# Kernel optimization log

Hardware: AMD Instinct MI355X
Metric: run time of the kernel (lower is better)

Reference implementation:

```python
import jax, jax.numpy as jnp
import numpy as np

MAX_NUM_CENTERS = 100
CENTER_IGNORE_PX = 3
SIGMA = 2.0   # center_gt_blur
KSIZE = 21    # GaussianLayer kernel size (ReflectionPad2d(10) + Conv2d(k=21))


def _gauss_kernel():
    r = KSIZE // 2
    x = jnp.arange(-r, r + 1, dtype=jnp.float32)
    g = jnp.exp(-0.5 * (x / SIGMA) ** 2)
    g = g / g.sum()
    return jnp.outer(g, g)  # [21,21], sums to 1 (matches scipy gaussian_filter of a delta)


def _gaussian_blur(x):
    # x: [B,H,W] -> depthwise 21x21 gaussian with reflect padding (GaussianLayer)
    r = KSIZE // 2
    k = _gauss_kernel()[None, None]  # [1,1,21,21]
    xp = jnp.pad(x[:, None], ((0, 0), (0, 0), (r, r), (r, r)), mode="reflect")
    y = jax.lax.conv_general_dilated(xp, k, (1, 1), "VALID",
                                     dimension_numbers=("NCHW", "OIHW", "NCHW"))
    return y[:, 0]


def setup_inputs() -> dict:
    key = jax.random.key(0)
    k1, k2 = jax.random.split(key)
    B, H, W = 8, 768, 768
    instances = jax.random.randint(k1, (B, 1, H, W), 0, MAX_NUM_CENTERS, dtype=jnp.int32)
    centers = jax.random.uniform(k2, (B, MAX_NUM_CENTERS, 2), dtype=jnp.float32) * (H - 1) + 1.0
    return {"instances": instances, "centers": centers}


def reference(instances, centers):
    B, _, H, W = instances.shape
    inst = instances[:, 0]                                # [B,H,W]
    col = jnp.arange(W, dtype=jnp.float32)                # xym_s[0][i,j] = j
    row = jnp.arange(H, dtype=jnp.float32)[:, None]       # xym_s[1][i,j] = i

    valid = inst > 0                                      # instance_mask
    has_inst = jnp.any(valid, axis=(1, 2)).astype(jnp.float32)  # len(unique)>1 gate

    # per-pixel nearest-center gather: center = centers[b, id-1]
    idx = jnp.clip(inst - 1, 0, MAX_NUM_CENTERS - 1)
    c = centers[jnp.arange(B)[:, None, None], idx]        # [B,H,W,2]
    gt_cx = jnp.where(valid, c[..., 1], -10000.0)         # gt_center_x (swapped coords)
    gt_cy = jnp.where(valid, c[..., 0], -10000.0)

    gt_X = gt_cx - row                                    # gt_center_x - xym_s[1]
    gt_Y = gt_cy - col                                    # gt_center_y - xym_s[0]

    near = (jnp.abs(gt_X) < CENTER_IGNORE_PX) & (jnp.abs(gt_Y) < CENTER_IGNORE_PX)
    # batches with no instances skip the block -> ignore stays all-ones
    ignore = jnp.where(has_inst[:, None, None] > 0, (~near).astype(jnp.float32), 1.0)

    m = valid.astype(jnp.float32)
    R = jnp.sqrt(gt_X ** 2 + gt_Y ** 2) * m
    theta_raw = jnp.arctan2(gt_Y, gt_X)
    theta = theta_raw * has_inst[:, None, None]           # skipped (zero) when no instances
    s = jnp.sin(theta_raw) * m
    cth = jnp.cos(theta_raw) * m
    M = jnp.sqrt(s ** 2 + cth ** 2)                       # == m, kept for faithfulness
    s = jnp.where(valid, s / jnp.maximum(M, 1e-12), 0.0)
    cth = jnp.where(valid, cth / jnp.maximum(M, 1e-12), 0.0)

    # gt_center_mask: zeros if no center-neighborhood pixels, else normalized blur
    blur = _gaussian_blur(1.0 - ignore)
    all_ones = jnp.all(ignore >= 1.0, axis=(1, 2))        # gt_center_mask.all()
    bmax = jnp.max(blur, axis=(1, 2), keepdims=True)
    cmask = jnp.where(all_ones[:, None, None], 0.0, blur / jnp.maximum(bmax, 1e-12))

    top = jnp.stack([R, theta, s, cth, ignore, cmask], axis=1)       # [B,6,H,W]
    mat = jnp.concatenate([top, jnp.zeros((B, 7, H, W), top.dtype)], axis=1)[:, :, None]
    # mat: [B,13,1,H,W]; channels 6..12 are zero (no orientation input)

    # gt_centers[id] = centers[b, id-1][[1,0]] for each instance id present
    present = jnp.zeros((B, MAX_NUM_CENTERS), dtype=bool).at[
        jnp.arange(B)[:, None], inst.reshape(B, -1)].set(True)
    swapped = centers[..., ::-1]
    gt_centers = jnp.zeros_like(centers).at[:, 1:, :].set(
        jnp.where(present[:, 1:, None], swapped[:, :-1, :], 0.0))

    return mat, gt_centers
```

## Files before the change

### kernel.cpp

```cpp
#include <hip/hip_runtime.h>
#include <math.h>

#define NB 8
#define NH 768
#define NW 768
#define NHW (NH*NW)
#define NCEN 100
#define NPIX (NB*NHW)
#define RAD 10
#define KS 21

#define SCAN_BLKS (NPIX / 4096)
#define BLKS_PER_B (NHW / 4096)
#define LIST_CAP 4096
#define QBLK_PER_B (NHW / 1024)
#define CAND_BLKS 96
#define FCAP 1024

#define HDR_HAS 0
#define HDR_CNT 8
#define HDR_BMAX 16
#define HDR_MASK 24
#define HDR_LIST 64

typedef float f4 __attribute__((ext_vector_type(4)));

__device__ const float g_G[KS] = {
    7.4335e-7f, 7.9919e-6f, 6.6915e-5f, 0.00043634f, 0.00221592f,
    0.00876415f, 0.02699548f, 0.06475880f, 0.12098536f, 0.17603266f,
    0.19947114f,
    0.17603266f, 0.12098536f, 0.06475880f, 0.02699548f, 0.00876415f,
    0.00221592f, 0.00043634f, 6.6915e-5f, 7.9919e-6f, 7.4335e-7f};

__device__ __forceinline__ float wfun(int p, int q, const float* __restrict__ g) {
    int d = p - q;
    float w = 0.f;
    if (d >= -RAD && d <= RAD) w = g[d + RAD];
    int a = p + q;
    if (q > 0 && a <= RAD) w += g[a + RAD];
    if (q < NH - 1 && a >= 2 * (NH - 1) - RAD) w += g[a - 2 * (NH - 1) + RAD];
    return w;
}

__device__ __forceinline__ float fatan2(float Y, float X) {
    float ax = fabsf(X), ay = fabsf(Y);
    float mx = fmaxf(ax, ay), mn = fminf(ax, ay);
    float a = mx > 0.f ? __fdividef(mn, mx) : 0.f;
    float ss = a * a;
    float r = fmaf(fmaf(fmaf(fmaf(fmaf(-0.01172120f, ss, 0.05265332f), ss,
                -0.11643287f), ss, 0.19354346f), ss, -0.33262347f), ss, 0.99997726f) * a;
    if (ay > ax) r = 1.57079637f - r;
    if (X < 0.f) r = 3.14159274f - r;
    return copysignf(r, Y);
}

__global__ void k_init(int* __restrict__ hdr) {
    if (threadIdx.x < 64) hdr[threadIdx.x] = 0;
}

__global__ __launch_bounds__(256) void k_scan(const int4* __restrict__ inst4,
                                              const float* __restrict__ centers,
                                              int* __restrict__ hdr) {
    __shared__ unsigned sm[4];
    __shared__ float2 s_c2[NCEN];
    int t = threadIdx.x;
    int blk = blockIdx.x;
    int b = blk / BLKS_PER_B;
    int lblk = blk - b * BLKS_PER_B;
    if (t < 4) sm[t] = 0;
    for (int k = t; k < NCEN; k += 256)
        s_c2[k] = ((const float2*)centers)[b * NCEN + k];
    __syncthreads();

    unsigned m0 = 0, m1 = 0, m2 = 0, m3 = 0;
    size_t base = (size_t)blk * 1024 + t;
    int ppb = lblk * 4096 + t * 4;
#pragma unroll
    for (int q = 0; q < 4; q++) {
        int4 v = inst4[base + (size_t)q * 256];
        int pp = ppb + q * 1024;
        int i = pp / NW;
        int j0 = pp - i * NW;
        int a[4] = {v.x, v.y, v.z, v.w};
#pragma unroll
        for (int e = 0; e < 4; e++) {
            int iv = a[e];
            if (iv > 0) {
                unsigned bit = 1u << (iv & 31);
                int w = iv >> 5;
                if (w == 0) m0 |= bit; else if (w == 1) m1 |= bit;
                else if (w == 2) m2 |= bit; else m3 |= bit;
                int idx = iv - 1;
                idx = idx > NCEN - 1 ? NCEN - 1 : idx;
                float2 c = s_c2[idx];
                if (fabsf(c.y - (float)i) < 3.f && fabsf(c.x - (float)(j0 + e)) < 3.f) {
                    int slot = atomicAdd(&hdr[HDR_CNT + b], 1);
                    if (slot < LIST_CAP)
                        hdr[HDR_LIST + b * LIST_CAP + slot] = (i << 16) | (j0 + e);
                }
            }
        }
    }
#pragma unroll
    for (int off = 32; off >= 1; off >>= 1) {
        m0 |= __shfl_xor(m0, off);
        m1 |= __shfl_xor(m1, off);
        m2 |= __shfl_xor(m2, off);
        m3 |= __shfl_xor(m3, off);
    }
    if ((t & 63) == 0) {
        if (m0) atomicOr(&sm[0], m0);
        if (m1) atomicOr(&sm[1], m1);
        if (m2) atomicOr(&sm[2], m2);
        if (m3) atomicOr(&sm[3], m3);
    }
    __syncthreads();
    if (t < 4) {
        unsigned v = sm[t];
        if (v) atomicOr((unsigned*)&hdr[HDR_MASK + b * 4 + t], v);
    }
}

__global__ __launch_bounds__(256) void k_bmax(const float* __restrict__ centers,
                                              int* __restrict__ hdr,
                                              float* __restrict__ gt) {
    __shared__ float s_g[KS];
    __shared__ int s_list[LIST_CAP];
    __shared__ float s_red[4];
    int t = threadIdx.x;
    int b = blockIdx.x / CAND_BLKS;
    int cb = blockIdx.x - b * CAND_BLKS;

    if (cb == 0) {
        const unsigned* pm = (const unsigned*)&hdr[HDR_MASK + b * 4];
        if (t < NCEN) {
            float vx = 0.f, vy = 0.f;
            if (t >= 1 && ((pm[t >> 5] >> (t & 31)) & 1u)) {
                vx = centers[(b * NCEN + (t - 1)) * 2 + 1];
                vy = centers[(b * NCEN + (t - 1)) * 2 + 0];
            }
            gt[(b * NCEN + t) * 2 + 0] = vx;
            gt[(b * NCEN + t) * 2 + 1] = vy;
        }
        if (t == 0) {
            unsigned any = (pm[0] & 0xFFFFFFFEu) | pm[1] | pm[2] | pm[3];
            hdr[HDR_HAS + b] = any ? 1 : 0;
        }
    }

    int M = hdr[HDR_CNT + b];
    M = M < LIST_CAP ? M : LIST_CAP;
    int total = M * (KS * KS);
    if (M == 0 || cb * 256 >= total) return;
    if (t < KS) s_g[t] = g_G[t];
    const int* gl = &hdr[HDR_LIST + b * LIST_CAP];
    for (int e = t; e < M; e += 256) s_list[e] = gl[e];
    __syncthreads();

    float lmax = 0.f;
    for (int c = cb * 256 + t; c < total; c += CAND_BLKS * 256) {
        int m = c / (KS * KS), r = c - m * (KS * KS);
        int e = s_list[m];
        int pi = (e >> 16) + r / KS - RAD;
        int pj = (e & 0xFFFF) + (r - (r / KS) * KS) - RAD;
        if (pi < 0 || pi >= NH || pj < 0 || pj >= NW) continue;
        float acc = 0.f;
        for (int m2 = 0; m2 < M; m2++) {
            int e2 = s_list[m2];
            float wi = wfun(pi, e2 >> 16, s_g);
            if (wi == 0.f) continue;
            acc += wi * wfun(pj, e2 & 0xFFFF, s_g);
        }
        lmax = fmaxf(lmax, acc);
    }
#pragma unroll
    for (int off = 32; off >= 1; off >>= 1) lmax = fmaxf(lmax, __shfl_down(lmax, off));
    if ((t & 63) == 0) s_red[t >> 6] = lmax;
    __syncthreads();
    if (t == 0) {
        float bmx = fmaxf(fmaxf(s_red[0], s_red[1]), fmaxf(s_red[2], s_red[3]));
        atomicMax((unsigned*)&hdr[HDR_BMAX + b], __float_as_uint(bmx));
    }
}

__global__ __launch_bounds__(256) void k_fused(const int* __restrict__ inst,
                                               const float* __restrict__ centers,
                                               const int* __restrict__ hdr,
                                               float* __restrict__ out) {
    __shared__ float s_cen[2 * NCEN];
    __shared__ float s_g[KS];
    __shared__ int s_fl[FCAP];
    __shared__ int s_fM;
    int t = threadIdx.x;
    int b = blockIdx.x / QBLK_PER_B;
    int qblk = blockIdx.x - b * QBLK_PER_B;

    int has = hdr[HDR_HAS + b];
    int M = hdr[HDR_CNT + b];
    M = M < LIST_CAP ? M : LIST_CAP;
    float bmx = __uint_as_float((unsigned)hdr[HDR_BMAX + b]);
    float sc = (has && M > 0) ? 1.f / fmaxf(bmx, 1e-12f) : 0.f;
    for (int k = t; k < 2 * NCEN; k += 256) s_cen[k] = centers[b * 2 * NCEN + k];
    if (t < KS) s_g[t] = g_G[t];
    if (t == 255) s_fM = 0;
    __syncthreads();

    int p0blk = qblk * 1024;
    int r0 = p0blk / NW;
    const int* gl = &hdr[HDR_LIST + b * LIST_CAP];
    for (int m = t; m < M; m += 256) {
        int e = gl[m];
        int qi = e >> 16;
        if (wfun(r0, qi, s_g) != 0.f || wfun(r0 + 1, qi, s_g) != 0.f) {
            int slot = atomicAdd(&s_fM, 1);
            if (slot < FCAP) s_fl[slot] = e;
        }
    }
    __syncthreads();
    int FM = s_fM < FCAP ? s_fM : FCAP;

    int p0 = p0blk + t * 4;
    int gi = p0 / NW;
    int gj0 = p0 - gi * NW;
    const int* instb = inst + (size_t)b * NHW;
    float* outb = out + (size_t)b * 13 * NHW;

    int4 ivv = *(const int4*)&instb[p0];
    int ia[4] = {ivv.x, ivv.y, ivv.z, ivv.w};
    f4 vR, vTh, vS, vC, vIg;
#pragma unroll
    for (int e = 0; e < 4; e++) {
        int iv = ia[e];
        bool valid = iv > 0;
        int idx = iv - 1;
        idx = idx < 0 ? 0 : idx;
        float cy = s_cen[2 * idx];
        float cx = s_cen[2 * idx + 1];
        float gcx = valid ? cx : -10000.f;
        float gcy = valid ? cy : -10000.f;
        float X = gcx - (float)gi;
        float Y = gcy - (float)(gj0 + e);
        bool near = (fabsf(X) < 3.f) && (fabsf(Y) < 3.f);
        vIg[e] = (has != 0) ? (near ? 0.f : 1.f) : 1.f;
        float m = valid ? 1.f : 0.f;
        float R2 = X * X + Y * Y;
        vR[e] = sqrtf(R2) * m;
        float rinv = R2 > 0.f ? rsqrtf(R2) : 0.f;
        vS[e] = valid ? Y * rinv : 0.f;
        vC[e] = valid ? (R2 > 0.f ? X * rinv : 1.f) : 0.f;
        float th = fatan2(Y, X);
        vTh[e] = (has != 0) ? th : 0.f;
    }

    f4 blur = {0.f, 0.f, 0.f, 0.f};
    for (int m = 0; m < FM; m++) {
        int e2 = s_fl[m];
        float wi = wfun(gi, e2 >> 16, s_g);
        if (wi == 0.f) continue;
        int qj = e2 & 0xFFFF;
#pragma unroll
        for (int e = 0; e < 4; e++) blur[e] += wi * wfun(gj0 + e, qj, s_g);
    }
    f4 vCm = blur * sc;

    __builtin_nontemporal_store(vR,  (f4*)&outb[(size_t)0 * NHW + p0]);
    __builtin_nontemporal_store(vTh, (f4*)&outb[(size_t)1 * NHW + p0]);
    __builtin_nontemporal_store(vS,  (f4*)&outb[(size_t)2 * NHW + p0]);
    __builtin_nontemporal_store(vC,  (f4*)&outb[(size_t)3 * NHW + p0]);
    __builtin_nontemporal_store(vIg, (f4*)&outb[(size_t)4 * NHW + p0]);
    __builtin_nontemporal_store(vCm, (f4*)&outb[(size_t)5 * NHW + p0]);
    f4 z = {0.f, 0.f, 0.f, 0.f};
#pragma unroll
    for (int ch = 6; ch < 13; ++ch)
        __builtin_nontemporal_store(z, (f4*)&outb[(size_t)ch * NHW + p0]);
}

extern "C" void kernel_launch(void* const* d_in, const int* in_sizes, int n_in,
                              void* d_out, int out_size, void* d_ws, size_t ws_size,
                              hipStream_t stream) {
    const int* inst = (const int*)d_in[0];
    const float* centers = (const float*)d_in[1];
    float* out = (float*)d_out;
    int* hdr = (int*)d_ws;
    float* gt = out + (size_t)NB * 13 * NHW;

    k_init<<<1, 64, 0, stream>>>(hdr);
    k_scan<<<SCAN_BLKS, 256, 0, stream>>>((const int4*)inst, centers, hdr);
    k_bmax<<<NB * CAND_BLKS, 256, 0, stream>>>(centers, hdr, gt);
    k_fused<<<NB * QBLK_PER_B, 256, 0, stream>>>(inst, centers, hdr, out);
}
```

Measured before the change: 275.4 us.

## Restructure pipeline: per-block candidate lists, u8 instance cache, zero-fill moved to mid kernel

```diff
diff --git a/kernel.cpp b/kernel.cpp
--- a/kernel.cpp
+++ b/kernel.cpp
@@ -12,16 +12,21 @@
 
 #define SCAN_BLKS (NPIX / 4096)
 #define BLKS_PER_B (NHW / 4096)
-#define LIST_CAP 4096
 #define QBLK_PER_B (NHW / 1024)
 #define CAND_BLKS 96
-#define FCAP 1024
-
-#define HDR_HAS 0
-#define HDR_CNT 8
-#define HDR_BMAX 16
-#define HDR_MASK 24
-#define HDR_LIST 64
+#define MID_BLKS 2048
+#define BSLOT 24
+#define BCAP 23
+#define GCAP 256
+#define FCAP 256
+
+#define OFF_MASKS 0
+#define OFF_BLIST 4608
+#define OFF_BMAXP 32256
+#define OFF_HAS   33024
+#define OFF_M     33032
+#define OFF_GLIST 33040
+#define WS_INTS   35088
 
 typedef float f4 __attribute__((ext_vector_type(4)));
 
@@ -54,20 +59,21 @@
     return copysignf(r, Y);
 }
 
-__global__ void k_init(int* __restrict__ hdr) {
-    if (threadIdx.x < 64) hdr[threadIdx.x] = 0;
-}
-
+template <bool U8>
 __global__ __launch_bounds__(256) void k_scan(const int4* __restrict__ inst4,
                                               const float* __restrict__ centers,
-                                              int* __restrict__ hdr) {
+                                              int* __restrict__ ws,
+                                              unsigned char* __restrict__ u8) {
     __shared__ unsigned sm[4];
     __shared__ float2 s_c2[NCEN];
+    __shared__ int s_loc[BCAP];
+    __shared__ int s_lcnt;
     int t = threadIdx.x;
     int blk = blockIdx.x;
     int b = blk / BLKS_PER_B;
     int lblk = blk - b * BLKS_PER_B;
     if (t < 4) sm[t] = 0;
+    if (t == 0) s_lcnt = 0;
     for (int k = t; k < NCEN; k += 256)
         s_c2[k] = ((const float2*)centers)[b * NCEN + k];
     __syncthreads();
@@ -81,6 +87,11 @@
         int pp = ppb + q * 1024;
         int i = pp / NW;
         int j0 = pp - i * NW;
+        if (U8) {
+            unsigned packed = ((unsigned)v.x & 255u) | (((unsigned)v.y & 255u) << 8) |
+                              (((unsigned)v.z & 255u) << 16) | (((unsigned)v.w & 255u) << 24);
+            *(unsigned*)&u8[(size_t)blk * 4096 + q * 1024 + t * 4] = packed;
+        }
         int a[4] = {v.x, v.y, v.z, v.w};
 #pragma unroll
         for (int e = 0; e < 4; e++) {
@@ -94,9 +105,8 @@
                 idx = idx > NCEN - 1 ? NCEN - 1 : idx;
                 float2 c = s_c2[idx];
                 if (fabsf(c.y - (float)i) < 3.f && fabsf(c.x - (float)(j0 + e)) < 3.f) {
-                    int slot = atomicAdd(&hdr[HDR_CNT + b], 1);
-                    if (slot < LIST_CAP)
-                        hdr[HDR_LIST + b * LIST_CAP + slot] = (i << 16) | (j0 + e);
+                    int slot = atomicAdd(&s_lcnt, 1);
+                    if (slot < BCAP) s_loc[slot] = (i << 16) | (j0 + e);
                 }
             }
         }
@@ -115,99 +125,138 @@
         if (m3) atomicOr(&sm[3], m3);
     }
     __syncthreads();
-    if (t < 4) {
-        unsigned v = sm[t];
-        if (v) atomicOr((unsigned*)&hdr[HDR_MASK + b * 4 + t], v);
-    }
-}
-
-__global__ __launch_bounds__(256) void k_bmax(const float* __restrict__ centers,
-                                              int* __restrict__ hdr,
-                                              float* __restrict__ gt) {
-    __shared__ float s_g[KS];
-    __shared__ int s_list[LIST_CAP];
-    __shared__ float s_red[4];
+    if (t < 4) ws[OFF_MASKS + blk * 4 + t] = (int)sm[t];
+    int cnt = s_lcnt < BCAP ? s_lcnt : BCAP;
+    int* slot = &ws[OFF_BLIST + blk * BSLOT];
+    if (t == 0) slot[0] = cnt;
+    if (t < cnt) slot[1 + t] = s_loc[t];
+}
+
+__global__ __launch_bounds__(256) void k_mid(const float* __restrict__ centers,
+                                             int* __restrict__ ws,
+                                             float* __restrict__ out) {
     int t = threadIdx.x;
-    int b = blockIdx.x / CAND_BLKS;
-    int cb = blockIdx.x - b * CAND_BLKS;
-
-    if (cb == 0) {
-        const unsigned* pm = (const unsigned*)&hdr[HDR_MASK + b * 4];
-        if (t < NCEN) {
-            float vx = 0.f, vy = 0.f;
-            if (t >= 1 && ((pm[t >> 5] >> (t & 31)) & 1u)) {
-                vx = centers[(b * NCEN + (t - 1)) * 2 + 1];
-                vy = centers[(b * NCEN + (t - 1)) * 2 + 0];
-            }
-            gt[(b * NCEN + t) * 2 + 0] = vx;
-            gt[(b * NCEN + t) * 2 + 1] = vy;
-        }
+    int g = blockIdx.x;
+
+    if (g < NB * CAND_BLKS) {
+        __shared__ float s_g[KS];
+        __shared__ int s_list[GCAP];
+        __shared__ int s_tot;
+        __shared__ unsigned s_m[4];
+        __shared__ float s_red[4];
+        int b = g / CAND_BLKS;
+        int cb = g - b * CAND_BLKS;
+        if (t < KS) s_g[t] = g_G[t];
+        if (t == 0) s_tot = 0;
+        if (t < 4) s_m[t] = 0;
+        __syncthreads();
+        if (t < BLKS_PER_B) {
+            const int* slot = &ws[OFF_BLIST + (b * BLKS_PER_B + t) * BSLOT];
+            int cnt = slot[0];
+            cnt = cnt < 0 ? 0 : (cnt > BCAP ? BCAP : cnt);
+            int basep = atomicAdd(&s_tot, cnt);
+            for (int i2 = 0; i2 < cnt; i2++) {
+                int s = basep + i2;
+                if (s < GCAP) s_list[s] = slot[1 + i2];
+            }
+            if (cb == 0) {
+                const unsigned* pm = (const unsigned*)&ws[OFF_MASKS + (b * BLKS_PER_B + t) * 4];
+                unsigned w0 = pm[0], w1 = pm[1], w2 = pm[2], w3 = pm[3];
+                if (w0) atomicOr(&s_m[0], w0);
+                if (w1) atomicOr(&s_m[1], w1);
+                if (w2) atomicOr(&s_m[2], w2);
+                if (w3) atomicOr(&s_m[3], w3);
+            }
+        }
+        __syncthreads();
+        int M = s_tot < GCAP ? s_tot : GCAP;
+
+        if (cb == 0) {
+            float* gt = out + (size_t)NB * 13 * NHW;
+            if (t < NCEN) {
+                float vx = 0.f, vy = 0.f;
+                if (t >= 1 && ((s_m[t >> 5] >> (t & 31)) & 1u)) {
+                    vx = centers[(b * NCEN + (t - 1)) * 2 + 1];
+                    vy = centers[(b * NCEN + (t - 1)) * 2 + 0];
+                }
+                gt[(b * NCEN + t) * 2 + 0] = vx;
+                gt[(b * NCEN + t) * 2 + 1] = vy;
+            }
+            if (t == 0) {
+                unsigned any = (s_m[0] & 0xFFFFFFFEu) | s_m[1] | s_m[2] | s_m[3];
+                ws[OFF_HAS + b] = any ? 1 : 0;
+                ws[OFF_M + b] = M;
+            }
+            for (int e = t; e < M; e += 256) ws[OFF_GLIST + b * GCAP + e] = s_list[e];
+        }
+
+        float lmax = 0.f;
+        int total = M * (KS * KS);
+        for (int c = cb * 256 + t; c < total; c += CAND_BLKS * 256) {
+            int m = c / (KS * KS), r = c - m * (KS * KS);
+            int e = s_list[m];
+            int pi = (e >> 16) + r / KS - RAD;
+            int pj = (e & 0xFFFF) + (r - (r / KS) * KS) - RAD;
+            if (pi < 0 || pi >= NH || pj < 0 || pj >= NW) continue;
+            float acc = 0.f;
+            for (int m2 = 0; m2 < M; m2++) {
+                int e2 = s_list[m2];
+                float wi = wfun(pi, e2 >> 16, s_g);
+                if (wi == 0.f) continue;
+                acc += wi * wfun(pj, e2 & 0xFFFF, s_g);
+            }
+            lmax = fmaxf(lmax, acc);
+        }
+#pragma unroll
+        for (int off = 32; off >= 1; off >>= 1) lmax = fmaxf(lmax, __shfl_down(lmax, off));
+        if ((t & 63) == 0) s_red[t >> 6] = lmax;
+        __syncthreads();
         if (t == 0) {
-            unsigned any = (pm[0] & 0xFFFFFFFEu) | pm[1] | pm[2] | pm[3];
-            hdr[HDR_HAS + b] = any ? 1 : 0;
-        }
-    }
-
-    int M = hdr[HDR_CNT + b];
-    M = M < LIST_CAP ? M : LIST_CAP;
-    int total = M * (KS * KS);
-    if (M == 0 || cb * 256 >= total) return;
-    if (t < KS) s_g[t] = g_G[t];
-    const int* gl = &hdr[HDR_LIST + b * LIST_CAP];
-    for (int e = t; e < M; e += 256) s_list[e] = gl[e];
-    __syncthreads();
-
-    float lmax = 0.f;
-    for (int c = cb * 256 + t; c < total; c += CAND_BLKS * 256) {
-        int m = c / (KS * KS), r = c - m * (KS * KS);
-        int e = s_list[m];
-        int pi = (e >> 16) + r / KS - RAD;
-        int pj = (e & 0xFFFF) + (r - (r / KS) * KS) - RAD;
-        if (pi < 0 || pi >= NH || pj < 0 || pj >= NW) continue;
-        float acc = 0.f;
-        for (int m2 = 0; m2 < M; m2++) {
-            int e2 = s_list[m2];
-            float wi = wfun(pi, e2 >> 16, s_g);
-            if (wi == 0.f) continue;
-            acc += wi * wfun(pj, e2 & 0xFFFF, s_g);
-        }
-        lmax = fmaxf(lmax, acc);
-    }
-#pragma unroll
-    for (int off = 32; off >= 1; off >>= 1) lmax = fmaxf(lmax, __shfl_down(lmax, off));
-    if ((t & 63) == 0) s_red[t >> 6] = lmax;
-    __syncthreads();
-    if (t == 0) {
-        float bmx = fmaxf(fmaxf(s_red[0], s_red[1]), fmaxf(s_red[2], s_red[3]));
-        atomicMax((unsigned*)&hdr[HDR_BMAX + b], __float_as_uint(bmx));
-    }
-}
-
+            float bmx = fmaxf(fmaxf(s_red[0], s_red[1]), fmaxf(s_red[2], s_red[3]));
+            ((float*)ws)[OFF_BMAXP + b * CAND_BLKS + cb] = bmx;
+        }
+    }
+
+    const int CH7Q = 7 * NHW / 4;
+    const int ZTOT = NB * CH7Q;
+    f4 z = {0.f, 0.f, 0.f, 0.f};
+    for (int zi = g * 256 + t; zi < ZTOT; zi += MID_BLKS * 256) {
+        int b2 = zi / CH7Q;
+        int rem = zi - b2 * CH7Q;
+        size_t off = (size_t)b2 * (13 * NHW / 4) + (6 * NHW / 4) + rem;
+        __builtin_nontemporal_store(z, (f4*)out + off);
+    }
+}
+
+template <bool U8>
 __global__ __launch_bounds__(256) void k_fused(const int* __restrict__ inst,
+                                               const unsigned char* __restrict__ u8,
                                                const float* __restrict__ centers,
-                                               const int* __restrict__ hdr,
+                                               const int* __restrict__ ws,
                                                float* __restrict__ out) {
     __shared__ float s_cen[2 * NCEN];
     __shared__ float s_g[KS];
     __shared__ int s_fl[FCAP];
     __shared__ int s_fM;
+    __shared__ unsigned s_bm;
     int t = threadIdx.x;
     int b = blockIdx.x / QBLK_PER_B;
     int qblk = blockIdx.x - b * QBLK_PER_B;
 
-    int has = hdr[HDR_HAS + b];
-    int M = hdr[HDR_CNT + b];
-    M = M < LIST_CAP ? M : LIST_CAP;
-    float bmx = __uint_as_float((unsigned)hdr[HDR_BMAX + b]);
-    float sc = (has && M > 0) ? 1.f / fmaxf(bmx, 1e-12f) : 0.f;
+    int has = ws[OFF_HAS + b];
+    int M = ws[OFF_M + b];
     for (int k = t; k < 2 * NCEN; k += 256) s_cen[k] = centers[b * 2 * NCEN + k];
     if (t < KS) s_g[t] = g_G[t];
     if (t == 255) s_fM = 0;
+    if (t == 254) s_bm = 0;
     __syncthreads();
+
+    if (t < CAND_BLKS)
+        atomicMax(&s_bm, __float_as_uint(((const float*)ws)[OFF_BMAXP + b * CAND_BLKS + t]));
 
     int p0blk = qblk * 1024;
     int r0 = p0blk / NW;
-    const int* gl = &hdr[HDR_LIST + b * LIST_CAP];
+    const int* gl = &ws[OFF_GLIST + b * GCAP];
     for (int m = t; m < M; m += 256) {
         int e = gl[m];
         int qi = e >> 16;
@@ -218,15 +267,22 @@
     }
     __syncthreads();
     int FM = s_fM < FCAP ? s_fM : FCAP;
+    float bmx = __uint_as_float(s_bm);
+    float sc = (has && M > 0) ? 1.f / fmaxf(bmx, 1e-12f) : 0.f;
 
     int p0 = p0blk + t * 4;
     int gi = p0 / NW;
     int gj0 = p0 - gi * NW;
-    const int* instb = inst + (size_t)b * NHW;
     float* outb = out + (size_t)b * 13 * NHW;
 
-    int4 ivv = *(const int4*)&instb[p0];
-    int ia[4] = {ivv.x, ivv.y, ivv.z, ivv.w};
+    int ia[4];
+    if (U8) {
+        unsigned v8 = *(const unsigned*)&u8[(size_t)b * NHW + p0];
+        ia[0] = v8 & 255; ia[1] = (v8 >> 8) & 255; ia[2] = (v8 >> 16) & 255; ia[3] = v8 >> 24;
+    } else {
+        int4 ivv = *(const int4*)&inst[(size_t)b * NHW + p0];
+        ia[0] = ivv.x; ia[1] = ivv.y; ia[2] = ivv.z; ia[3] = ivv.w;
+    }
     f4 vR, vTh, vS, vC, vIg;
 #pragma unroll
     for (int e = 0; e < 4; e++) {
@@ -269,10 +325,6 @@
     __builtin_nontemporal_store(vC,  (f4*)&outb[(size_t)3 * NHW + p0]);
     __builtin_nontemporal_store(vIg, (f4*)&outb[(size_t)4 * NHW + p0]);
     __builtin_nontemporal_store(vCm, (f4*)&outb[(size_t)5 * NHW + p0]);
-    f4 z = {0.f, 0.f, 0.f, 0.f};
-#pragma unroll
-    for (int ch = 6; ch < 13; ++ch)
-        __builtin_nontemporal_store(z, (f4*)&outb[(size_t)ch * NHW + p0]);
 }
 
 extern "C" void kernel_launch(void* const* d_in, const int* in_sizes, int n_in,
@@ -281,11 +333,17 @@
     const int* inst = (const int*)d_in[0];
     const float* centers = (const float*)d_in[1];
     float* out = (float*)d_out;
-    int* hdr = (int*)d_ws;
-    float* gt = out + (size_t)NB * 13 * NHW;
-
-    k_init<<<1, 64, 0, stream>>>(hdr);
-    k_scan<<<SCAN_BLKS, 256, 0, stream>>>((const int4*)inst, centers, hdr);
-    k_bmax<<<NB * CAND_BLKS, 256, 0, stream>>>(centers, hdr, gt);
-    k_fused<<<NB * QBLK_PER_B, 256, 0, stream>>>(inst, centers, hdr, out);
-}
+    int* ws = (int*)d_ws;
+    unsigned char* u8 = (unsigned char*)d_ws + (size_t)WS_INTS * 4;
+    bool use_u8 = ws_size >= (size_t)WS_INTS * 4 + (size_t)NPIX;
+
+    if (use_u8) {
+        k_scan<true><<<SCAN_BLKS, 256, 0, stream>>>((const int4*)inst, centers, ws, u8);
+        k_mid<<<MID_BLKS, 256, 0, stream>>>(centers, ws, out);
+        k_fused<true><<<NB * QBLK_PER_B, 256, 0, stream>>>(inst, u8, centers, ws, out);
+    } else {
+        k_scan<false><<<SCAN_BLKS, 256, 0, stream>>>((const int4*)inst, centers, ws, u8);
+        k_mid<<<MID_BLKS, 256, 0, stream>>>(centers, ws, out);
+        k_fused<false><<<NB * QBLK_PER_B, 256, 0, stream>>>(inst, u8, centers, ws, out);
+    }
+}
```

Result: no change. 270.1 us (-1.9%).

## Merge scan and blur-max into one kernel, move zero-channel stores into it

Applied to the files above, without the earlier changes.

```diff
diff --git a/kernel.cpp b/kernel.cpp
--- a/kernel.cpp
+++ b/kernel.cpp
@@ -10,18 +10,26 @@
 #define RAD 10
 #define KS 21
 
-#define SCAN_BLKS (NPIX / 4096)
+#define MAIN_BLKS (NPIX / 4096)
 #define BLKS_PER_B (NHW / 4096)
-#define LIST_CAP 4096
-#define QBLK_PER_B (NHW / 1024)
-#define CAND_BLKS 96
-#define FCAP 1024
-
-#define HDR_HAS 0
-#define HDR_CNT 8
-#define HDR_BMAX 16
-#define HDR_MASK 24
-#define HDR_LIST 64
+#define TAILS 64
+#define CANDS_PER_B 8
+#define ZPB 7168
+#define ZIT (ZPB/256)
+#define GCAP 256
+#define FCAP 256
+#define NPQ 3
+#define FBLK_PX (NPQ*1024)
+#define QBLK3_PER_B (NHW / FBLK_PX)
+
+#define STORE(v, p) (*(p) = (v))
+
+#define OFF_CNT   0
+#define OFF_MASK  8
+#define OFF_DONE  40
+#define OFF_HAS   41
+#define OFF_BMAXP 64
+#define OFF_GLIST 128
 
 typedef float f4 __attribute__((ext_vector_type(4)));
 
@@ -54,20 +62,25 @@
     return copysignf(r, Y);
 }
 
-__global__ void k_init(int* __restrict__ hdr) {
-    if (threadIdx.x < 64) hdr[threadIdx.x] = 0;
-}
-
-__global__ __launch_bounds__(256) void k_scan(const int4* __restrict__ inst4,
+__global__ void k_init(int* __restrict__ ws) {
+    if (threadIdx.x < 64) ws[threadIdx.x] = 0;
+}
+
+__global__ __launch_bounds__(256) void k_main(const int4* __restrict__ inst4,
                                               const float* __restrict__ centers,
-                                              int* __restrict__ hdr) {
-    __shared__ unsigned sm[4];
+                                              int* __restrict__ ws,
+                                              float* __restrict__ out) {
     __shared__ float2 s_c2[NCEN];
+    __shared__ float s_g[KS];
+    __shared__ int s_list[GCAP];
+    __shared__ float s_red[4];
+    __shared__ int s_slot;
     int t = threadIdx.x;
     int blk = blockIdx.x;
     int b = blk / BLKS_PER_B;
     int lblk = blk - b * BLKS_PER_B;
-    if (t < 4) sm[t] = 0;
+
+    if (t < KS) s_g[t] = g_G[t];
     for (int k = t; k < NCEN; k += 256)
         s_c2[k] = ((const float2*)centers)[b * NCEN + k];
     __syncthreads();
@@ -94,9 +107,9 @@
                 idx = idx > NCEN - 1 ? NCEN - 1 : idx;
                 float2 c = s_c2[idx];
                 if (fabsf(c.y - (float)i) < 3.f && fabsf(c.x - (float)(j0 + e)) < 3.f) {
-                    int slot = atomicAdd(&hdr[HDR_CNT + b], 1);
-                    if (slot < LIST_CAP)
-                        hdr[HDR_LIST + b * LIST_CAP + slot] = (i << 16) | (j0 + e);
+                    int slot = atomicAdd(&ws[OFF_CNT + b], 1);
+                    if (slot < GCAP)
+                        ws[OFF_GLIST + b * GCAP + slot] = (i << 16) | (j0 + e);
                 }
             }
         }
@@ -109,170 +122,163 @@
         m3 |= __shfl_xor(m3, off);
     }
     if ((t & 63) == 0) {
-        if (m0) atomicOr(&sm[0], m0);
-        if (m1) atomicOr(&sm[1], m1);
-        if (m2) atomicOr(&sm[2], m2);
-        if (m3) atomicOr(&sm[3], m3);
-    }
-    __syncthreads();
-    if (t < 4) {
-        unsigned v = sm[t];
-        if (v) atomicOr((unsigned*)&hdr[HDR_MASK + b * 4 + t], v);
-    }
-}
-
-__global__ __launch_bounds__(256) void k_bmax(const float* __restrict__ centers,
-                                              int* __restrict__ hdr,
-                                              float* __restrict__ gt) {
-    __shared__ float s_g[KS];
-    __shared__ int s_list[LIST_CAP];
-    __shared__ float s_red[4];
-    int t = threadIdx.x;
-    int b = blockIdx.x / CAND_BLKS;
-    int cb = blockIdx.x - b * CAND_BLKS;
-
-    if (cb == 0) {
-        const unsigned* pm = (const unsigned*)&hdr[HDR_MASK + b * 4];
-        if (t < NCEN) {
-            float vx = 0.f, vy = 0.f;
-            if (t >= 1 && ((pm[t >> 5] >> (t & 31)) & 1u)) {
-                vx = centers[(b * NCEN + (t - 1)) * 2 + 1];
-                vy = centers[(b * NCEN + (t - 1)) * 2 + 0];
-            }
-            gt[(b * NCEN + t) * 2 + 0] = vx;
-            gt[(b * NCEN + t) * 2 + 1] = vy;
-        }
+        unsigned* pm = (unsigned*)&ws[OFF_MASK + b * 4];
+        if (m0) atomicOr(&pm[0], m0);
+        if (m1) atomicOr(&pm[1], m1);
+        if (m2) atomicOr(&pm[2], m2);
+        if (m3) atomicOr(&pm[3], m3);
+    }
+    __syncthreads();
+    __threadfence();
+    if (t == 0) s_slot = atomicAdd(&ws[OFF_DONE], 1);
+    __syncthreads();
+    int slot = s_slot;
+
+    if (slot >= MAIN_BLKS - TAILS) {
+        int k = slot - (MAIN_BLKS - TAILS);
+        int tb = k >> 3;
+        int cb = k & 7;
         if (t == 0) {
-            unsigned any = (pm[0] & 0xFFFFFFFEu) | pm[1] | pm[2] | pm[3];
-            hdr[HDR_HAS + b] = any ? 1 : 0;
-        }
-    }
-
-    int M = hdr[HDR_CNT + b];
-    M = M < LIST_CAP ? M : LIST_CAP;
-    int total = M * (KS * KS);
-    if (M == 0 || cb * 256 >= total) return;
-    if (t < KS) s_g[t] = g_G[t];
-    const int* gl = &hdr[HDR_LIST + b * LIST_CAP];
-    for (int e = t; e < M; e += 256) s_list[e] = gl[e];
-    __syncthreads();
-
-    float lmax = 0.f;
-    for (int c = cb * 256 + t; c < total; c += CAND_BLKS * 256) {
-        int m = c / (KS * KS), r = c - m * (KS * KS);
-        int e = s_list[m];
-        int pi = (e >> 16) + r / KS - RAD;
-        int pj = (e & 0xFFFF) + (r - (r / KS) * KS) - RAD;
-        if (pi < 0 || pi >= NH || pj < 0 || pj >= NW) continue;
-        float acc = 0.f;
-        for (int m2 = 0; m2 < M; m2++) {
-            int e2 = s_list[m2];
-            float wi = wfun(pi, e2 >> 16, s_g);
-            if (wi == 0.f) continue;
-            acc += wi * wfun(pj, e2 & 0xFFFF, s_g);
-        }
-        lmax = fmaxf(lmax, acc);
-    }
-#pragma unroll
-    for (int off = 32; off >= 1; off >>= 1) lmax = fmaxf(lmax, __shfl_down(lmax, off));
-    if ((t & 63) == 0) s_red[t >> 6] = lmax;
-    __syncthreads();
-    if (t == 0) {
-        float bmx = fmaxf(fmaxf(s_red[0], s_red[1]), fmaxf(s_red[2], s_red[3]));
-        atomicMax((unsigned*)&hdr[HDR_BMAX + b], __float_as_uint(bmx));
-    }
+            while (atomicAdd(&ws[OFF_DONE], 0) < MAIN_BLKS)
+                __builtin_amdgcn_s_sleep(8);
+        }
+        __syncthreads();
+        __threadfence();
+        int M = ws[OFF_CNT + tb];
+        M = M < GCAP ? M : GCAP;
+        for (int e = t; e < M; e += 256) s_list[e] = ws[OFF_GLIST + tb * GCAP + e];
+        __syncthreads();
+
+        if (cb == 0) {
+            const unsigned* pm = (const unsigned*)&ws[OFF_MASK + tb * 4];
+            float* gt = out + (size_t)NB * 13 * NHW;
+            if (t < NCEN) {
+                float vx = 0.f, vy = 0.f;
+                if (t >= 1 && ((pm[t >> 5] >> (t & 31)) & 1u)) {
+                    vx = centers[(tb * NCEN + (t - 1)) * 2 + 1];
+                    vy = centers[(tb * NCEN + (t - 1)) * 2 + 0];
+                }
+                gt[(tb * NCEN + t) * 2 + 0] = vx;
+                gt[(tb * NCEN + t) * 2 + 1] = vy;
+            }
+            if (t == 0) {
+                unsigned any = (pm[0] & 0xFFFFFFFEu) | pm[1] | pm[2] | pm[3];
+                ws[OFF_HAS + tb] = any ? 1 : 0;
+            }
+        }
+
+        float lmax = 0.f;
+        int total = M * (KS * KS);
+        for (int c = cb * 256 + t; c < total; c += CANDS_PER_B * 256) {
+            int m = c / (KS * KS), r = c - m * (KS * KS);
+            int e = s_list[m];
+            int pi = (e >> 16) + r / KS - RAD;
+            int pj = (e & 0xFFFF) + (r - (r / KS) * KS) - RAD;
+            if (pi < 0 || pi >= NH || pj < 0 || pj >= NW) continue;
+            float acc = 0.f;
+            for (int m2 = 0; m2 < M; m2++) {
+                int e2 = s_list[m2];
+                float wi = wfun(pi, e2 >> 16, s_g);
+                if (wi == 0.f) continue;
+                acc += wi * wfun(pj, e2 & 0xFFFF, s_g);
+            }
+            lmax = fmaxf(lmax, acc);
+        }
+#pragma unroll
+        for (int off = 32; off >= 1; off >>= 1) lmax = fmaxf(lmax, __shfl_down(lmax, off));
+        if ((t & 63) == 0) s_red[t >> 6] = lmax;
+        __syncthreads();
+        if (t == 0) {
+            float bmx = fmaxf(fmaxf(s_red[0], s_red[1]), fmaxf(s_red[2], s_red[3]));
+            ((float*)ws)[OFF_BMAXP + tb * CANDS_PER_B + cb] = bmx;
+        }
+    }
+
+    const f4 z = {0.f, 0.f, 0.f, 0.f};
+    f4* dst = (f4*)(out + (size_t)b * 13 * NHW + (size_t)6 * NHW) + lblk * ZPB + t;
+#pragma unroll
+    for (int it = 0; it < ZIT; ++it) STORE(z, dst + it * 256);
 }
 
 __global__ __launch_bounds__(256) void k_fused(const int* __restrict__ inst,
                                                const float* __restrict__ centers,
-                                               const int* __restrict__ hdr,
+                                               const int* __restrict__ ws,
                                                float* __restrict__ out) {
     __shared__ float s_cen[2 * NCEN];
     __shared__ float s_g[KS];
     __shared__ int s_fl[FCAP];
     __shared__ int s_fM;
+    __shared__ unsigned s_bm;
     int t = threadIdx.x;
-    int b = blockIdx.x / QBLK_PER_B;
-    int qblk = blockIdx.x - b * QBLK_PER_B;
-
-    int has = hdr[HDR_HAS + b];
-    int M = hdr[HDR_CNT + b];
-    M = M < LIST_CAP ? M : LIST_CAP;
-    float bmx = __uint_as_float((unsigned)hdr[HDR_BMAX + b]);
-    float sc = (has && M > 0) ? 1.f / fmaxf(bmx, 1e-12f) : 0.f;
+    int b = blockIdx.x / QBLK3_PER_B;
+    int qblk = blockIdx.x - b * QBLK3_PER_B;
+    int has = ws[OFF_HAS + b];
+    int M = ws[OFF_CNT + b];
+    M = M < GCAP ? M : GCAP;
     for (int k = t; k < 2 * NCEN; k += 256) s_cen[k] = centers[b * 2 * NCEN + k];
     if (t < KS) s_g[t] = g_G[t];
     if (t == 255) s_fM = 0;
-    __syncthreads();
-
-    int p0blk = qblk * 1024;
-    int r0 = p0blk / NW;
-    const int* gl = &hdr[HDR_LIST + b * LIST_CAP];
+    if (t == 254) s_bm = 0;
+    __syncthreads();
+    if (t < CANDS_PER_B)
+        atomicMax(&s_bm, __float_as_uint(((const float*)ws)[OFF_BMAXP + b * CANDS_PER_B + t]));
+    int p0blk = qblk * FBLK_PX;
+    int r0 = qblk * 4;
+    const int* gl = &ws[OFF_GLIST + b * GCAP];
     for (int m = t; m < M; m += 256) {
         int e = gl[m];
         int qi = e >> 16;
-        if (wfun(r0, qi, s_g) != 0.f || wfun(r0 + 1, qi, s_g) != 0.f) {
+        if (qi >= r0 - RAD && qi <= r0 + 3 + RAD) {
             int slot = atomicAdd(&s_fM, 1);
             if (slot < FCAP) s_fl[slot] = e;
         }
     }
     __syncthreads();
     int FM = s_fM < FCAP ? s_fM : FCAP;
-
-    int p0 = p0blk + t * 4;
-    int gi = p0 / NW;
-    int gj0 = p0 - gi * NW;
-    const int* instb = inst + (size_t)b * NHW;
+    float sc = (has && M > 0) ? 1.f / fmaxf(__uint_as_float(s_bm), 1e-12f) : 0.f;
     float* outb = out + (size_t)b * 13 * NHW;
-
-    int4 ivv = *(const int4*)&instb[p0];
-    int ia[4] = {ivv.x, ivv.y, ivv.z, ivv.w};
-    f4 vR, vTh, vS, vC, vIg;
-#pragma unroll
-    for (int e = 0; e < 4; e++) {
-        int iv = ia[e];
-        bool valid = iv > 0;
-        int idx = iv - 1;
-        idx = idx < 0 ? 0 : idx;
-        float cy = s_cen[2 * idx];
-        float cx = s_cen[2 * idx + 1];
-        float gcx = valid ? cx : -10000.f;
-        float gcy = valid ? cy : -10000.f;
-        float X = gcx - (float)gi;
-        float Y = gcy - (float)(gj0 + e);
-        bool near = (fabsf(X) < 3.f) && (fabsf(Y) < 3.f);
-        vIg[e] = (has != 0) ? (near ? 0.f : 1.f) : 1.f;
-        float m = valid ? 1.f : 0.f;
-        float R2 = X * X + Y * Y;
-        vR[e] = sqrtf(R2) * m;
-        float rinv = R2 > 0.f ? rsqrtf(R2) : 0.f;
-        vS[e] = valid ? Y * rinv : 0.f;
-        vC[e] = valid ? (R2 > 0.f ? X * rinv : 1.f) : 0.f;
-        float th = fatan2(Y, X);
-        vTh[e] = (has != 0) ? th : 0.f;
-    }
-
-    f4 blur = {0.f, 0.f, 0.f, 0.f};
-    for (int m = 0; m < FM; m++) {
-        int e2 = s_fl[m];
-        float wi = wfun(gi, e2 >> 16, s_g);
-        if (wi == 0.f) continue;
-        int qj = e2 & 0xFFFF;
-#pragma unroll
-        for (int e = 0; e < 4; e++) blur[e] += wi * wfun(gj0 + e, qj, s_g);
-    }
-    f4 vCm = blur * sc;
-
-    __builtin_nontemporal_store(vR,  (f4*)&outb[(size_t)0 * NHW + p0]);
-    __builtin_nontemporal_store(vTh, (f4*)&outb[(size_t)1 * NHW + p0]);
-    __builtin_nontemporal_store(vS,  (f4*)&outb[(size_t)2 * NHW + p0]);
-    __builtin_nontemporal_store(vC,  (f4*)&outb[(size_t)3 * NHW + p0]);
-    __builtin_nontemporal_store(vIg, (f4*)&outb[(size_t)4 * NHW + p0]);
-    __builtin_nontemporal_store(vCm, (f4*)&outb[(size_t)5 * NHW + p0]);
-    f4 z = {0.f, 0.f, 0.f, 0.f};
-#pragma unroll
-    for (int ch = 6; ch < 13; ++ch)
-        __builtin_nontemporal_store(z, (f4*)&outb[(size_t)ch * NHW + p0]);
+    for (int qq = 0; qq < NPQ; ++qq) {
+        int p0 = p0blk + qq * 1024 + t * 4;
+        int gi = p0 / NW, gj0 = p0 - (p0 / NW) * NW;
+        int4 ivv = *(const int4*)&inst[(size_t)b * NHW + p0];
+        int ia[4] = {ivv.x, ivv.y, ivv.z, ivv.w};
+        f4 vR, vTh, vS, vC, vIg;
+#pragma unroll
+        for (int e = 0; e < 4; e++) {
+            int iv = ia[e];
+            bool valid = iv > 0;
+            int idx = iv - 1;
+            idx = idx < 0 ? 0 : idx;
+            float cy = s_cen[2 * idx], cx = s_cen[2 * idx + 1];
+            float X = (valid ? cx : -10000.f) - (float)gi;
+            float Y = (valid ? cy : -10000.f) - (float)(gj0 + e);
+            bool near = (fabsf(X) < 3.f) && (fabsf(Y) < 3.f);
+            vIg[e] = near ? 0.f : 1.f;
+            float m = valid ? 1.f : 0.f;
+            float R2 = X * X + Y * Y;
+            vR[e] = sqrtf(R2) * m;
+            float rinv = R2 > 0.f ? rsqrtf(R2) : 0.f;
+            vS[e] = valid ? Y * rinv : 0.f;
+            vC[e] = valid ? (R2 > 0.f ? X * rinv : 1.f) : 0.f;
+            vTh[e] = has ? fatan2(Y, X) : 0.f;
+        }
+        f4 blur = {0.f, 0.f, 0.f, 0.f};
+        for (int m = 0; m < FM; m++) {
+            int e2 = s_fl[m];
+            float wi = wfun(gi, e2 >> 16, s_g);
+            if (wi == 0.f) continue;
+            int qj = e2 & 0xFFFF;
+#pragma unroll
+            for (int e = 0; e < 4; e++) blur[e] += wi * wfun(gj0 + e, qj, s_g);
+        }
+        f4 vCm = blur * sc;
+        STORE(vR,  (f4*)&outb[(size_t)0 * NHW + p0]);
+        STORE(vTh, (f4*)&outb[(size_t)1 * NHW + p0]);
+        STORE(vS,  (f4*)&outb[(size_t)2 * NHW + p0]);
+        STORE(vC,  (f4*)&outb[(size_t)3 * NHW + p0]);
+        STORE(vIg, (f4*)&outb[(size_t)4 * NHW + p0]);
+        STORE(vCm, (f4*)&outb[(size_t)5 * NHW + p0]);
+    }
 }
 
 extern "C" void kernel_launch(void* const* d_in, const int* in_sizes, int n_in,
@@ -281,11 +287,9 @@
     const int* inst = (const int*)d_in[0];
     const float* centers = (const float*)d_in[1];
     float* out = (float*)d_out;
-    int* hdr = (int*)d_ws;
-    float* gt = out + (size_t)NB * 13 * NHW;
-
-    k_init<<<1, 64, 0, stream>>>(hdr);
-    k_scan<<<SCAN_BLKS, 256, 0, stream>>>((const int4*)inst, centers, hdr);
-    k_bmax<<<NB * CAND_BLKS, 256, 0, stream>>>(centers, hdr, gt);
-    k_fused<<<NB * QBLK_PER_B, 256, 0, stream>>>(inst, centers, hdr, out);
-}
+    int* ws = (int*)d_ws;
+
+    k_init<<<1, 64, 0, stream>>>(ws);
+    k_main<<<MAIN_BLKS, 256, 0, stream>>>((const int4*)inst, centers, ws, out);
+    k_fused<<<NB * QBLK3_PER_B, 256, 0, stream>>>(inst, centers, ws, out);
+}
```

After: 504.9 us. 83.3% more time.
